# Kernel tuning notes

Hardware: AMD Instinct MI355X
Metric: run time of the kernel (lower is better)

## Reference

```python
import jax, jax.numpy as jnp
import numpy as np

N_QUBITS = 20
N_PART = 10  # log2(out_features=1024)
W_MUL = (2.0 ** 0.5) * (5.0 ** -0.5)  # he_std * lrmul with gain=sqrt(2), lrmul=1

_H = (jnp.array([[1.0, 1.0], [1.0, -1.0]], dtype=jnp.complex64) / jnp.sqrt(jnp.array(2.0, jnp.float32)))


def _rx(theta):
    c = jnp.cos(theta * 0.5).astype(jnp.complex64)
    s = (-1j * jnp.sin(theta * 0.5)).astype(jnp.complex64)
    return jnp.stack([jnp.stack([c, s]), jnp.stack([s, c])])


def _ry(theta):
    c = jnp.cos(theta * 0.5).astype(jnp.complex64)
    s = jnp.sin(theta * 0.5).astype(jnp.complex64)
    return jnp.stack([jnp.stack([c, -s]), jnp.stack([s, c])])


def _rz(theta):
    e = jnp.exp(-0.5j * theta.astype(jnp.complex64))
    z = jnp.zeros((), jnp.complex64)
    return jnp.stack([jnp.stack([e, z]), jnp.stack([z, jnp.conj(e)])])


def _apply_1q(state, gate, q):
    # Apply 2x2 gate on qubit q (qubit 0 = most significant bit, matching kron order).
    s = state.reshape(2 ** q, 2, -1)
    return jnp.einsum('ab,ibj->iaj', gate, s).reshape(-1)


def _apply_cnot(state, c, t, n):
    a, b = (c, t) if c < t else (t, c)
    s = state.reshape(2 ** a, 2, 2 ** (b - a - 1), 2, 2 ** (n - b - 1))
    if c < t:
        # control at axis 1; after slicing, target is axis 2
        s = s.at[:, 1].set(jnp.flip(s[:, 1], axis=2))
    else:
        # control at axis 3; after slicing, target is axis 1
        s = s.at[:, :, :, 1].set(jnp.flip(s[:, :, :, 1], axis=1))
    return s.reshape(-1)


def setup_inputs() -> dict:
    key = jax.random.key(0)
    kx, kw = jax.random.split(key)
    x = jax.random.normal(kx, (1, N_QUBITS), dtype=jnp.float32)
    weight = jax.random.uniform(kw, (3 * N_QUBITS,), dtype=jnp.float32,
                                minval=0.0, maxval=2.0 * np.pi)
    return {"x": x, "weight": weight}


def reference(x, weight):
    n = N_QUBITS
    xq = jnp.squeeze(x)  # (n_qubits,)
    state = jnp.zeros(2 ** n, dtype=jnp.complex64).at[0].set(1.0 + 0j)
    # encoding layer: H, ry(arctan(x)), rz(arctan(x^2)) on each qubit
    for q in range(n):
        state = _apply_1q(state, _H, q)
        state = _apply_1q(state, _ry(jnp.arctan(xq[q])), q)
        state = _apply_1q(state, _rz(jnp.arctan(xq[q] * xq[q])), q)
    # variational layer: ring of CNOTs (q -> q+1, q -> q+2), then rx,rz,rx
    w = weight * W_MUL
    for q in range(n):
        state = _apply_cnot(state, q, (q + 1) % n, n)
        state = _apply_cnot(state, q, (q + 2) % n, n)
    for q in range(n):
        state = _apply_1q(state, _rx(w[3 * q + 0]), q)
        state = _apply_1q(state, _rz(w[3 * q + 1]), q)
        state = _apply_1q(state, _rx(w[3 * q + 2]), q)
    # partial measurement of the first N_PART (most significant) qubits:
    # marginalize |amp|^2 over the remaining qubits
    probs = (jnp.abs(state) ** 2).astype(jnp.float32)
    hidden = probs.reshape(2 ** N_PART, -1).sum(axis=1)
    return hidden[None, :]  # (1, 2**N_PART)
```

## Files before the change

kernel.cpp:

```cpp
#include <hip/hip_runtime.h>
#include <cstdint>


#define NQ      20
#define NPART   10
#define NH      1024
#define BLOCK   256
#define NBLOCKS 256

struct MaskArg { uint32_t m[NQ]; };

__device__ __forceinline__ float2 cmul(float2 a, float2 b) {
    return make_float2(fmaf(a.x, b.x, -a.y * b.y), fmaf(a.x, b.y, a.y * b.x));
}
__device__ __forceinline__ float2 cadd(float2 a, float2 b) {
    return make_float2(a.x + b.x, a.y + b.y);
}

__global__ __launch_bounds__(BLOCK) void qulinear_kernel(
        const float* __restrict__ x, const float* __restrict__ w,
        float* __restrict__ out, MaskArg masks) {
    __shared__ float2   v[NQ][2];
    __shared__ float2   U[NPART][2][2];
    __shared__ uint32_t stab[16];
    __shared__ float    hid[4][NH];

    const int tid = threadIdx.x;

    if (tid < NQ) {
        float xq = x[tid];
        float th = atanf(xq);
        float ph = atanf(xq * xq);
        float c, s, cp, sp;
        __sincosf(0.5f * th, &s, &c);
        __sincosf(0.5f * ph, &sp, &cp);
        float a = (c - s) * 0.70710678118654752f;
        float b = (c + s) * 0.70710678118654752f;
        v[tid][0] = make_float2(a * cp, -a * sp);
        v[tid][1] = make_float2(b * cp,  b * sp);
    }
    if (tid < NPART) {
        const float WM = 0.63245553203367590f;
        float a0 = w[3 * tid + 0] * WM;
        float a1 = w[3 * tid + 1] * WM;
        float a2 = w[3 * tid + 2] * WM;
        float c0, s0, c1, s1, c2, s2;
        __sincosf(0.5f * a0, &s0, &c0);
        __sincosf(0.5f * a1, &s1, &c1);
        __sincosf(0.5f * a2, &s2, &c2);
        float2 e0 = make_float2(c1, -s1), e1 = make_float2(c1, s1);
        float2 m00 = cmul(e0, make_float2(c0, 0.f));
        float2 m01 = cmul(e0, make_float2(0.f, -s0));
        float2 m10 = cmul(e1, make_float2(0.f, -s0));
        float2 m11 = cmul(e1, make_float2(c0, 0.f));
        float2 r00 = make_float2(c2, 0.f), r01 = make_float2(0.f, -s2);
        U[tid][0][0] = cadd(cmul(r00, m00), cmul(r01, m10));
        U[tid][0][1] = cadd(cmul(r00, m01), cmul(r01, m11));
        U[tid][1][0] = cadd(cmul(r01, m00), cmul(r00, m10));
        U[tid][1][1] = cadd(cmul(r01, m01), cmul(r00, m11));
    }
    if (tid < 16) {
        uint32_t y = (uint32_t)tid << 16;
        uint32_t s = 0;
        #pragma unroll
        for (int q = 0; q < NQ; ++q)
            s |= (uint32_t)(__popc(masks.m[q] & y) & 1) << q;
        stab[tid] = s;
    }
    __syncthreads();

    const int wave = tid >> 6;
    const int lane = tid & 63;
    const uint32_t l = (uint32_t)(blockIdx.x * 4 + wave);

    const uint32_t y0 = ((uint32_t)lane << NPART) | l;
    uint32_t sbase = 0;
    #pragma unroll
    for (int q = 0; q < NQ; ++q)
        sbase |= (uint32_t)(__popc(masks.m[q] & y0) & 1) << q;

    uint32_t s[16];
    #pragma unroll
    for (int r = 0; r < 16; ++r) s[r] = sbase ^ stab[r];

    float2 amp[16];
    #pragma unroll
    for (int r = 0; r < 16; ++r) amp[r] = make_float2(1.f, 0.f);

    #pragma unroll 4
    for (int q = 0; q < NQ; ++q) {
        float2 v0 = v[q][0], v1 = v[q][1];
        #pragma unroll
        for (int r = 0; r < 16; ++r) {
            bool b = (s[r] >> q) & 1u;
            float2 sel = make_float2(b ? v1.x : v0.x, b ? v1.y : v0.y);
            amp[r] = cmul(amp[r], sel);
        }
    }

    #pragma unroll
    for (int p = 0; p < 6; ++p) {
        const int lm = 1 << p;
        const bool bit = (lane & lm) != 0;
        float2 g00 = U[9 - p][0][0], g01 = U[9 - p][0][1];
        float2 g10 = U[9 - p][1][0], g11 = U[9 - p][1][1];
        float2 ga = bit ? g11 : g00;
        float2 gb = bit ? g10 : g01;
        #pragma unroll
        for (int r = 0; r < 16; ++r) {
            float2 mine = amp[r];
            float2 oth = make_float2(__shfl_xor(mine.x, lm, 64),
                                     __shfl_xor(mine.y, lm, 64));
            amp[r] = cadd(cmul(ga, mine), cmul(gb, oth));
        }
    }

    #pragma unroll
    for (int p = 6; p < 10; ++p) {
        const int pb = p - 6;
        float2 g00 = U[9 - p][0][0], g01 = U[9 - p][0][1];
        float2 g10 = U[9 - p][1][0], g11 = U[9 - p][1][1];
        #pragma unroll
        for (int j = 0; j < 8; ++j) {
            int lo = j & ((1 << pb) - 1);
            int r0 = ((j >> pb) << (pb + 1)) | lo;
            int r1 = r0 | (1 << pb);
            float2 a = amp[r0], b = amp[r1];
            amp[r0] = cadd(cmul(g00, a), cmul(g01, b));
            amp[r1] = cadd(cmul(g10, a), cmul(g11, b));
        }
    }

    #pragma unroll
    for (int r = 0; r < 16; ++r) {
        int h = (r << 6) | lane;
        hid[wave][h] = fmaf(amp[r].x, amp[r].x, amp[r].y * amp[r].y);
    }
    __syncthreads();

    #pragma unroll
    for (int k = 0; k < NH / BLOCK; ++k) {
        int h = tid + k * BLOCK;
        float acc = hid[0][h] + hid[1][h] + hid[2][h] + hid[3][h];
        atomicAdd(&out[h], acc);
    }
}

extern "C" void kernel_launch(void* const* d_in, const int* in_sizes, int n_in,
                              void* d_out, int out_size, void* d_ws, size_t ws_size,
                              hipStream_t stream) {
    const float* x = (const float*)d_in[0];
    const float* w = (const float*)d_in[1];
    float* out = (float*)d_out;

    MaskArg ma;
    {
        uint32_t M[NQ];
        for (int q = 0; q < NQ; ++q) M[q] = 1u << q;
        for (int q = NQ - 1; q >= 0; --q) {
            M[(q + 2) % NQ] ^= M[q];
            M[(q + 1) % NQ] ^= M[q];
        }
        for (int q = 0; q < NQ; ++q) {
            uint32_t im = 0;
            for (int j = 0; j < NQ; ++j)
                if ((M[q] >> j) & 1) im |= 1u << (NQ - 1 - j);
            ma.m[q] = im;
        }
    }

    hipMemsetAsync(d_out, 0, (size_t)out_size * sizeof(float), stream);
    qulinear_kernel<<<NBLOCKS, BLOCK, 0, stream>>>(x, w, out, ma);
}
```

Before: 74.04 us.

## Split per-wave work across four waves with LDS gate exchange and sliced atomics

Each block now handles one low-index group, with the four waves each taking a quarter of the 16 amplitude rows, so the grid grows from 256 to 1024 blocks and each thread keeps 4 amplitudes instead of 16. The two high qubits spanning waves are combined through a shared-memory exchange using a precomputed 4x4 tensor-product gate. Output accumulation moves to 32 workspace slices via global atomics, followed by a separate reduce kernel. The aim is more parallelism and lower register pressure, at the cost of an extra kernel launch, a workspace memset and more global atomics.

```diff
diff --git a/kernel.cpp b/kernel.cpp
--- a/kernel.cpp
+++ b/kernel.cpp
@@ -6,7 +6,7 @@
 #define NPART   10
 #define NH      1024
 #define BLOCK   256
-#define NBLOCKS 256
+#define NSLICE  32
 
 struct MaskArg { uint32_t m[NQ]; };
 
@@ -17,13 +17,12 @@
     return make_float2(a.x + b.x, a.y + b.y);
 }
 
-__global__ __launch_bounds__(BLOCK) void qulinear_kernel(
+__global__ __launch_bounds__(BLOCK, 4) void qulinear_kernel(
         const float* __restrict__ x, const float* __restrict__ w,
-        float* __restrict__ out, MaskArg masks) {
-    __shared__ float2   v[NQ][2];
-    __shared__ float2   U[NPART][2][2];
-    __shared__ uint32_t stab[16];
-    __shared__ float    hid[4][NH];
+        float* __restrict__ ws, MaskArg masks) {
+    __shared__ float2 v[NQ][2];
+    __shared__ float2 U[NPART][2][2];
+    __shared__ float2 ex[4][4][64];
 
     const int tid = threadIdx.x;
 
@@ -59,43 +58,62 @@
         U[tid][1][0] = cadd(cmul(r01, m00), cmul(r00, m10));
         U[tid][1][1] = cadd(cmul(r01, m01), cmul(r00, m11));
     }
-    if (tid < 16) {
-        uint32_t y = (uint32_t)tid << 16;
-        uint32_t s = 0;
-        #pragma unroll
-        for (int q = 0; q < NQ; ++q)
-            s |= (uint32_t)(__popc(masks.m[q] & y) & 1) << q;
-        stab[tid] = s;
-    }
     __syncthreads();
 
-    const int wave = tid >> 6;
+    const int wq   = tid >> 6;
     const int lane = tid & 63;
-    const uint32_t l = (uint32_t)(blockIdx.x * 4 + wave);
+    const uint32_t l = blockIdx.x;
 
-    const uint32_t y0 = ((uint32_t)lane << NPART) | l;
-    uint32_t sbase = 0;
+    const uint32_t y0 = ((uint32_t)lane << NPART) | l | ((uint32_t)wq << 18);
+    uint32_t sbase = 0, d16 = 0, d17 = 0;
     #pragma unroll
-    for (int q = 0; q < NQ; ++q)
+    for (int q = 0; q < NQ; ++q) {
         sbase |= (uint32_t)(__popc(masks.m[q] & y0) & 1) << q;
+        d16   |= (uint32_t)((masks.m[q] >> 16) & 1u) << q;
+        d17   |= (uint32_t)((masks.m[q] >> 17) & 1u) << q;
+    }
+    uint32_t s[4];
+    s[0] = sbase; s[1] = sbase ^ d16; s[2] = sbase ^ d17; s[3] = sbase ^ d16 ^ d17;
 
-    uint32_t s[16];
+    float2 g[4];
     #pragma unroll
-    for (int r = 0; r < 16; ++r) s[r] = sbase ^ stab[r];
+    for (int j = 0; j < 4; ++j)
+        g[j] = cmul(U[0][wq >> 1][j >> 1], U[1][wq & 1][j & 1]);
 
-    float2 amp[16];
+    float2 amp[4];
     #pragma unroll
-    for (int r = 0; r < 16; ++r) amp[r] = make_float2(1.f, 0.f);
+    for (int r = 0; r < 4; ++r) amp[r] = make_float2(1.f, 0.f);
 
-    #pragma unroll 4
+    #pragma unroll
     for (int q = 0; q < NQ; ++q) {
         float2 v0 = v[q][0], v1 = v[q][1];
         #pragma unroll
-        for (int r = 0; r < 16; ++r) {
+        for (int r = 0; r < 4; ++r) {
             bool b = (s[r] >> q) & 1u;
             float2 sel = make_float2(b ? v1.x : v0.x, b ? v1.y : v0.y);
             amp[r] = cmul(amp[r], sel);
         }
+    }
+
+    {
+        float2 g00 = U[3][0][0], g01 = U[3][0][1], g10 = U[3][1][0], g11 = U[3][1][1];
+        float2 a, b;
+        a = amp[0]; b = amp[1];
+        amp[0] = cadd(cmul(g00, a), cmul(g01, b));
+        amp[1] = cadd(cmul(g10, a), cmul(g11, b));
+        a = amp[2]; b = amp[3];
+        amp[2] = cadd(cmul(g00, a), cmul(g01, b));
+        amp[3] = cadd(cmul(g10, a), cmul(g11, b));
+    }
+    {
+        float2 g00 = U[2][0][0], g01 = U[2][0][1], g10 = U[2][1][0], g11 = U[2][1][1];
+        float2 a, b;
+        a = amp[0]; b = amp[2];
+        amp[0] = cadd(cmul(g00, a), cmul(g01, b));
+        amp[2] = cadd(cmul(g10, a), cmul(g11, b));
+        a = amp[1]; b = amp[3];
+        amp[1] = cadd(cmul(g00, a), cmul(g01, b));
+        amp[3] = cadd(cmul(g10, a), cmul(g11, b));
     }
 
     #pragma unroll
@@ -107,7 +125,7 @@
         float2 ga = bit ? g11 : g00;
         float2 gb = bit ? g10 : g01;
         #pragma unroll
-        for (int r = 0; r < 16; ++r) {
+        for (int r = 0; r < 4; ++r) {
             float2 mine = amp[r];
             float2 oth = make_float2(__shfl_xor(mine.x, lm, 64),
                                      __shfl_xor(mine.y, lm, 64));
@@ -116,34 +134,32 @@
     }
 
     #pragma unroll
-    for (int p = 6; p < 10; ++p) {
-        const int pb = p - 6;
-        float2 g00 = U[9 - p][0][0], g01 = U[9 - p][0][1];
-        float2 g10 = U[9 - p][1][0], g11 = U[9 - p][1][1];
-        #pragma unroll
-        for (int j = 0; j < 8; ++j) {
-            int lo = j & ((1 << pb) - 1);
-            int r0 = ((j >> pb) << (pb + 1)) | lo;
-            int r1 = r0 | (1 << pb);
-            float2 a = amp[r0], b = amp[r1];
-            amp[r0] = cadd(cmul(g00, a), cmul(g01, b));
-            amp[r1] = cadd(cmul(g10, a), cmul(g11, b));
-        }
+    for (int r = 0; r < 4; ++r) ex[wq][r][lane] = amp[r];
+    __syncthreads();
+    #pragma unroll
+    for (int r = 0; r < 4; ++r) {
+        float2 acc = cmul(g[0], ex[0][r][lane]);
+        acc = cadd(acc, cmul(g[1], ex[1][r][lane]));
+        acc = cadd(acc, cmul(g[2], ex[2][r][lane]));
+        acc = cadd(acc, cmul(g[3], ex[3][r][lane]));
+        amp[r] = acc;
     }
 
+    float* wsp = ws + (size_t)(blockIdx.x & (NSLICE - 1)) * NH;
     #pragma unroll
-    for (int r = 0; r < 16; ++r) {
-        int h = (r << 6) | lane;
-        hid[wave][h] = fmaf(amp[r].x, amp[r].x, amp[r].y * amp[r].y);
+    for (int r = 0; r < 4; ++r) {
+        int h = (wq << 8) | (r << 6) | lane;
+        atomicAdd(&wsp[h], fmaf(amp[r].x, amp[r].x, amp[r].y * amp[r].y));
     }
-    __syncthreads();
+}
 
+__global__ __launch_bounds__(BLOCK) void reduce_kernel(
+        const float* __restrict__ ws, float* __restrict__ out) {
+    int h = blockIdx.x * BLOCK + threadIdx.x;
+    float acc = 0.f;
     #pragma unroll
-    for (int k = 0; k < NH / BLOCK; ++k) {
-        int h = tid + k * BLOCK;
-        float acc = hid[0][h] + hid[1][h] + hid[2][h] + hid[3][h];
-        atomicAdd(&out[h], acc);
-    }
+    for (int s = 0; s < NSLICE; ++s) acc += ws[s * NH + h];
+    out[h] = acc;
 }
 
 extern "C" void kernel_launch(void* const* d_in, const int* in_sizes, int n_in,
@@ -169,6 +185,7 @@
         }
     }
 
-    hipMemsetAsync(d_out, 0, (size_t)out_size * sizeof(float), stream);
-    qulinear_kernel<<<NBLOCKS, BLOCK, 0, stream>>>(x, w, out, ma);
+    hipMemsetAsync(d_ws, 0, (size_t)NSLICE * NH * sizeof(float), stream);
+    qulinear_kernel<<<NH, BLOCK, 0, stream>>>(x, w, (float*)d_ws, ma);
+    reduce_kernel<<<NH / BLOCK, BLOCK, 0, stream>>>((const float*)d_ws, out);
 }
```

Result: faster. 66.88 us (-9.7%).
